# Kernel tuning notes

Hardware: AMD Instinct MI355X
Metric: run time of the kernel (lower is better)

## Reference

```python
import jax, jax.numpy as jnp
import numpy as np

B, N, C = 8, 2048, 512  # batch, points, channels; dk == C


def _mlp(x, W, b):
    # torch MLP helper = Linear followed by ReLU (even on the last layer)
    return jax.nn.relu(x @ W + b)


def setup_inputs() -> dict:
    key = jax.random.key(0)
    ks = jax.random.split(key, 5)
    s = 1.0 / np.sqrt(C)
    return {
        "x": jax.random.normal(ks[0], (B, N, C), dtype=jnp.float32),
        "Wh": jax.random.normal(ks[1], (C, C), dtype=jnp.float32) * s,
        "bh": jnp.zeros((C,), dtype=jnp.float32),
        "Wl": jax.random.normal(ks[2], (C, C), dtype=jnp.float32) * s,
        "bl": jnp.zeros((C,), dtype=jnp.float32),
        "Wg": jax.random.normal(ks[3], (C, C), dtype=jnp.float32) * s,
        "bg": jnp.zeros((C,), dtype=jnp.float32),
        "Wm": jax.random.normal(ks[4], (C, C), dtype=jnp.float32) * s,
        "bm": jnp.zeros((C,), dtype=jnp.float32),
    }


def reference(x, Wh, bh, Wl, bl, Wg, bg, Wm, bm):
    h = _mlp(x, Wh, bh)                      # [B, N, dk] (torch transposes; folded into einsum)
    l = _mlp(x, Wl, bl)                      # [B, N, dk]
    scores = jnp.einsum("bnd,bmd->bnm", l, h)  # [B, N, N]
    attn = jax.nn.softmax(scores, axis=-1)
    g = _mlp(x, Wg, bg)                      # [B, N, C]
    out = x + jnp.einsum("bnm,bmc->bnc", attn, g)
    return _mlp(out, Wm, bm)
```

## Files before the change

### kernel.cpp

```cpp
#include <hip/hip_runtime.h>


typedef __attribute__((ext_vector_type(4))) float f32x4;
typedef __attribute__((ext_vector_type(8))) short s16x8;
typedef __attribute__((ext_vector_type(4))) short s16x4;
typedef __attribute__((ext_vector_type(8))) _Float16 f16x8;
typedef __attribute__((ext_vector_type(4))) _Float16 f16x4;
typedef __attribute__((ext_vector_type(2))) unsigned u32x2;

typedef unsigned int u32;
typedef __attribute__((address_space(1))) const u32 gu32;
typedef __attribute__((address_space(3))) u32 lu32;

__device__ __forceinline__ void gload16(const short* g, short* l) {
  __builtin_amdgcn_global_load_lds((gu32*)g, (lu32*)l, 16, 0, 0);
}

__device__ __forceinline__ short f2h(float f) {
  _Float16 h = (_Float16)f;
  return __builtin_bit_cast(short, h);
}

__device__ __forceinline__ unsigned pk2h(float a, float b) {
  return __builtin_bit_cast(unsigned, __builtin_amdgcn_cvt_pkrtz(a, b));
}

#define MFMA(a, b, c) __builtin_amdgcn_mfma_f32_16x16x32_f16(a, b, c, 0, 0, 0)
#define MFMA16(a, b, c) __builtin_amdgcn_mfma_f32_16x16x16f16(a, b, c, 0, 0, 0)

#define BAR_KEEP2()                                          \
  do {                                                       \
    asm volatile("s_waitcnt vmcnt(2)" ::: "memory");         \
    __builtin_amdgcn_s_barrier();                            \
    __builtin_amdgcn_sched_barrier(0);                       \
  } while (0)
#define BAR_ALL()                                            \
  do {                                                       \
    asm volatile("s_waitcnt vmcnt(0)" ::: "memory");         \
    __builtin_amdgcn_s_barrier();                            \
    __builtin_amdgcn_sched_barrier(0);                       \
  } while (0)


__global__ __launch_bounds__(256) void conv_x_kernel(const float* __restrict__ x,
                                                     short* __restrict__ xb) {
  int i = blockIdx.x * 256 + threadIdx.x;
  const float4* xv = (const float4*)x;
  float4 a = xv[2 * i], b = xv[2 * i + 1];
  s16x8 o;
  o[0] = f2h(a.x); o[1] = f2h(a.y); o[2] = f2h(a.z); o[3] = f2h(a.w);
  o[4] = f2h(b.x); o[5] = f2h(b.y); o[6] = f2h(b.z); o[7] = f2h(b.w);
  ((s16x8*)xb)[i] = o;
}

__global__ __launch_bounds__(256) void conv_w_kernel(const float* __restrict__ Wh,
                                                     const float* __restrict__ Wl,
                                                     const float* __restrict__ Wg,
                                                     const float* __restrict__ Wm,
                                                     short* __restrict__ Wt) {
  int idx = blockIdx.x * 256 + threadIdx.x;
  int k = idx & 511, n = (idx >> 9) & 511, w = idx >> 18;
  const float* W = (w == 0) ? Wh : (w == 1) ? Wl : (w == 2) ? Wg : Wm;
  Wt[idx] = f2h(W[k * 512 + n]);
}


__global__ __launch_bounds__(256) void mlp3_kernel(const short* __restrict__ A,
                                                   const short* __restrict__ Wt_all,
                                                   const float* __restrict__ bh,
                                                   const float* __restrict__ bl,
                                                   const float* __restrict__ bg,
                                                   short* __restrict__ h,
                                                   short* __restrict__ l,
                                                   short* __restrict__ gT) {
  int z = blockIdx.z;
  const short* Wt = Wt_all + z * 262144;
  const float* bias = (z == 0) ? bh : (z == 1) ? bl : bg;

  __shared__ __align__(16) short lds_a[128 * 40];
  __shared__ __align__(16) short lds_b[128 * 40];
  int tid = threadIdx.x, lane = tid & 63, w = tid >> 6;
  int wm = w >> 1, wn = w & 1;
  int bm = blockIdx.x * 128, bn = blockIdx.y * 128;

  f32x4 acc[4][4];
#pragma unroll
  for (int mi = 0; mi < 4; ++mi)
#pragma unroll
    for (int ni = 0; ni < 4; ++ni) acc[mi][ni] = (f32x4){0.f, 0.f, 0.f, 0.f};

  for (int k0 = 0; k0 < 512; k0 += 32) {
#pragma unroll
    for (int it = 0; it < 2; ++it) {
      int chunk = tid + it * 256;
      int row = chunk >> 2, c8 = (chunk & 3) * 8;
      *(s16x8*)&lds_a[row * 40 + c8] =
          *(const s16x8*)&A[(size_t)(bm + row) * 512 + k0 + c8];
      *(s16x8*)&lds_b[row * 40 + c8] =
          *(const s16x8*)&Wt[(bn + row) * 512 + k0 + c8];
    }
    __syncthreads();
    f16x8 af[4], bfr[4];
#pragma unroll
    for (int mi = 0; mi < 4; ++mi)
      af[mi] = *(const f16x8*)&lds_a[(wm * 64 + mi * 16 + (lane & 15)) * 40 +
                                     (lane >> 4) * 8];
#pragma unroll
    for (int ni = 0; ni < 4; ++ni)
      bfr[ni] = *(const f16x8*)&lds_b[(wn * 64 + ni * 16 + (lane & 15)) * 40 +
                                      (lane >> 4) * 8];
#pragma unroll
    for (int mi = 0; mi < 4; ++mi)
#pragma unroll
      for (int ni = 0; ni < 4; ++ni) acc[mi][ni] = MFMA(af[mi], bfr[ni], acc[mi][ni]);
    __syncthreads();
  }

#pragma unroll
  for (int mi = 0; mi < 4; ++mi)
#pragma unroll
    for (int ni = 0; ni < 4; ++ni) {
      int col = bn + wn * 64 + ni * 16 + (lane & 15);
      float bv = bias[col];
#pragma unroll
      for (int r = 0; r < 4; ++r) {
        int row = bm + wm * 64 + mi * 16 + (lane >> 4) * 4 + r;
        float v = fmaxf(acc[mi][ni][r] + bv, 0.0f);
        short o = f2h(v);
        if (z == 0) h[(size_t)row * 512 + col] = o;
        else if (z == 1) l[(size_t)row * 512 + col] = o;
        else {
          int bb = row >> 11, mm = row & 2047;
          gT[((size_t)bb * 512 + col) * 2048 + mm] = o;
        }
      }
    }
}


__global__ __launch_bounds__(512, 1) void attn_split_kernel(
    const short* __restrict__ lmat, const short* __restrict__ hmat,
    const short* __restrict__ gT,
    short* __restrict__ OA, short* __restrict__ OB,
    float2* __restrict__ mlA, float2* __restrict__ mlB) {
  __shared__ __align__(16) short kbuf[3][8192];
  __shared__ __align__(16) short gbuf[2][8192];
  int tid = threadIdx.x, lane = tid & 63, w = tid >> 6;
  int b = blockIdx.x & 7;
  int idx = blockIdx.x >> 3;
  int qt = idx >> 1, sp = idx & 1;
  int q0 = qt * 128 + w * 16;
  int keybase = sp * 1024;
  const short* lb = lmat + (size_t)b * 2048 * 512;
  const short* hb = hmat + (size_t)b * 2048 * 512;
  const short* gb = gT + (size_t)b * 512 * 2048;
  short* Op = sp ? OB : OA;
  float2* ml = sp ? mlB : mlA;

  int r0 = lane & 15, g = lane >> 4;

  f16x8 qf[16];
  {
    int q = q0 + r0;
#pragma unroll
    for (int ks = 0; ks < 16; ++ks)
      qf[ks] = *(const f16x8*)&lb[(size_t)q * 512 + ks * 32 + g * 8];
  }
  f32x4 accO[32];
#pragma unroll
  for (int i = 0; i < 32; ++i) accO[i] = (f32x4){0.f, 0.f, 0.f, 0.f};
  float mrun = -3e38f, lsumL = 0.f;

  auto stageK = [&](int t) {
    int key0 = keybase + t * 16;
    short* kd = &kbuf[t % 3][0];
#pragma unroll
    for (int j = 0; j < 2; ++j) {
      int wl = w * 2 + j;
      gload16(hb + (size_t)(key0 + wl) * 512 + (((lane * 16) ^ ((wl & 7) << 4)) >> 1),
              kd + wl * 512);
    }
  };
  auto stageG = [&](int t) {
    int key0 = keybase + t * 16;
    short* gd = &gbuf[t & 1][0];
#pragma unroll
    for (int j = 0; j < 2; ++j) {
      int wl = w * 2 + j;
      int c = wl * 32 + (lane >> 1);
      int half = (lane & 1) ^ ((lane >> 3) & 1);
      gload16(gb + (size_t)c * 2048 + key0 + half * 8, gd + wl * 512);
    }
  };
  auto QK = [&](int t, f32x4& o) {
    const short* kb = &kbuf[t % 3][0];
#pragma unroll
    for (int ks = 0; ks < 16; ++ks) {
      f16x8 kf = *(const f16x8*)&kb[(r0 * 512 + ks * 32 + g * 8) ^ ((r0 & 7) << 3)];
      o = MFMA(kf, qf[ks], o);
    }
  };

  stageK(0); stageK(1); stageG(0); stageK(2);
  BAR_KEEP2();
  f32x4 sc = {0.f, 0.f, 0.f, 0.f};
  QK(0, sc);
  BAR_KEEP2();

  int goff = r0 * 16 + (((g >> 1) ^ ((r0 >> 2) & 1)) << 3) + ((g & 1) << 2);

  for (int t = 0; t < 64; ++t) {
    if (t < 63) stageG(t + 1);
    if (t < 61) stageK(t + 3);

    f32x4 sn = {0.f, 0.f, 0.f, 0.f};
    if (t < 63) {
      __builtin_amdgcn_s_setprio(1);
      QK(t + 1, sn);
      __builtin_amdgcn_s_setprio(0);
    }

    float m2 = fmaxf(fmaxf(sc[0], sc[1]), fmaxf(sc[2], sc[3]));
    m2 = fmaxf(m2, __shfl_xor(m2, 16));
    m2 = fmaxf(m2, __shfl_xor(m2, 32));
    bool ok = (m2 <= mrun + 8.0f);
    if (!__all((int)ok)) {
      float mnew = fmaxf(mrun, m2);
      float s = __expf(mrun - mnew);
      mrun = mnew;
      lsumL *= s;
#pragma unroll
      for (int nf = 0; nf < 32; ++nf) accO[nf] *= s;
    }
    float p0 = __expf(sc[0] - mrun), p1 = __expf(sc[1] - mrun);
    float p2 = __expf(sc[2] - mrun), p3 = __expf(sc[3] - mrun);
    lsumL += (p0 + p1) + (p2 + p3);

    u32x2 pw = {pk2h(p0, p1), pk2h(p2, p3)};
    f16x4 pfrag = __builtin_bit_cast(f16x4, pw);

    const short* gp = &gbuf[t & 1][goff];
    __builtin_amdgcn_s_setprio(1);
#pragma unroll
    for (int nf = 0; nf < 32; ++nf) {
      f16x4 gf = *(const f16x4*)&gp[nf * 256];
      accO[nf] = MFMA16(gf, pfrag, accO[nf]);
    }
    __builtin_amdgcn_s_setprio(0);

    if (t < 61) BAR_KEEP2(); else BAR_ALL();
    sc = sn;
  }

  float ls = lsumL;
  ls += __shfl_xor(ls, 16);
  ls += __shfl_xor(ls, 32);
  float inv = 1.0f / ls;
  int q = q0 + r0;
#pragma unroll
  for (int nf = 0; nf < 32; ++nf) {
    s16x4 o;
    o[0] = f2h(accO[nf][0] * inv);
    o[1] = f2h(accO[nf][1] * inv);
    o[2] = f2h(accO[nf][2] * inv);
    o[3] = f2h(accO[nf][3] * inv);
    *(s16x4*)&Op[((size_t)b * 2048 + q) * 512 + nf * 16 + g * 4] = o;
  }
  if (g == 0) ml[(size_t)b * 2048 + q] = make_float2(mrun, ls);
}


__global__ __launch_bounds__(256) void final_gemm_kernel(
    const short* __restrict__ OA, const short* __restrict__ OB,
    const float2* __restrict__ mlA, const float2* __restrict__ mlB,
    const float* __restrict__ x, const short* __restrict__ Wt,
    const float* __restrict__ bias, float* __restrict__ out) {
  __shared__ __align__(16) short lds_a[64 * 40];
  __shared__ __align__(16) short lds_b[512 * 40];
  int tid = threadIdx.x, lane = tid & 63, w = tid >> 6;
  int bm = blockIdx.x * 64;

  int arow = tid >> 2, ac8 = (tid & 3) * 8;
  int grow = bm + arow;
  float2 a2 = mlA[grow], b2 = mlB[grow];
  float ms = fmaxf(a2.x, b2.x);
  float wA = __expf(a2.x - ms) * a2.y;
  float wB = __expf(b2.x - ms) * b2.y;
  float winv = 1.0f / (wA + wB);
  wA *= winv; wB *= winv;

  f32x4 acc[32];
#pragma unroll
  for (int i = 0; i < 32; ++i) acc[i] = (f32x4){0.f, 0.f, 0.f, 0.f};

  for (int k0 = 0; k0 < 512; k0 += 32) {
    {
      size_t base = (size_t)grow * 512 + k0 + ac8;
      f16x8 oa = *(const f16x8*)&OA[base];
      f16x8 ob = *(const f16x8*)&OB[base];
      float4 x0 = *(const float4*)&x[base];
      float4 x1 = *(const float4*)&x[base + 4];
      s16x8 av;
      av[0] = f2h((float)oa[0] * wA + (float)ob[0] * wB + x0.x);
      av[1] = f2h((float)oa[1] * wA + (float)ob[1] * wB + x0.y);
      av[2] = f2h((float)oa[2] * wA + (float)ob[2] * wB + x0.z);
      av[3] = f2h((float)oa[3] * wA + (float)ob[3] * wB + x0.w);
      av[4] = f2h((float)oa[4] * wA + (float)ob[4] * wB + x1.x);
      av[5] = f2h((float)oa[5] * wA + (float)ob[5] * wB + x1.y);
      av[6] = f2h((float)oa[6] * wA + (float)ob[6] * wB + x1.z);
      av[7] = f2h((float)oa[7] * wA + (float)ob[7] * wB + x1.w);
      *(s16x8*)&lds_a[arow * 40 + ac8] = av;
    }
#pragma unroll
    for (int it = 0; it < 8; ++it) {
      int chunk = tid + it * 256;
      int row = chunk >> 2, c8 = (chunk & 3) * 8;
      *(s16x8*)&lds_b[row * 40 + c8] =
          *(const s16x8*)&Wt[(size_t)row * 512 + k0 + c8];
    }
    __syncthreads();
    f16x8 af = *(const f16x8*)&lds_a[(w * 16 + (lane & 15)) * 40 + (lane >> 4) * 8];
#pragma unroll
    for (int nf = 0; nf < 32; ++nf) {
      f16x8 bf = *(const f16x8*)&lds_b[(nf * 16 + (lane & 15)) * 40 + (lane >> 4) * 8];
      acc[nf] = MFMA(af, bf, acc[nf]);
    }
    __syncthreads();
  }

#pragma unroll
  for (int nf = 0; nf < 32; ++nf) {
    int col = nf * 16 + (lane & 15);
    float bv = bias[col];
#pragma unroll
    for (int r = 0; r < 4; ++r) {
      int row = bm + w * 16 + (lane >> 4) * 4 + r;
      out[(size_t)row * 512 + col] = fmaxf(acc[nf][r] + bv, 0.0f);
    }
  }
}


extern "C" void kernel_launch(void* const* d_in, const int* in_sizes, int n_in,
                              void* d_out, int out_size, void* d_ws, size_t ws_size,
                              hipStream_t stream) {
  const float* x  = (const float*)d_in[0];
  const float* Wh = (const float*)d_in[1];
  const float* bh = (const float*)d_in[2];
  const float* Wl = (const float*)d_in[3];
  const float* bl = (const float*)d_in[4];
  const float* Wg = (const float*)d_in[5];
  const float* bg = (const float*)d_in[6];
  const float* Wm = (const float*)d_in[7];
  const float* bm = (const float*)d_in[8];

  char* ws = (char*)d_ws;
  const size_t SZ = 16777216;
  short*  xb  = (short*)(ws + 0 * SZ);
  short*  h   = (short*)(ws + 1 * SZ);
  short*  l   = (short*)(ws + 2 * SZ);
  short*  gT  = (short*)(ws + 3 * SZ);
  short*  OB  = (short*)(ws + 4 * SZ);
  short*  Wt  = (short*)(ws + 5 * SZ);
  float2* mlA = (float2*)(ws + 5 * SZ + 2097152);
  float2* mlB = (float2*)(ws + 5 * SZ + 2097152 + 131072);

  conv_x_kernel<<<4096, 256, 0, stream>>>(x, xb);
  conv_w_kernel<<<4096, 256, 0, stream>>>(Wh, Wl, Wg, Wm, Wt);
  mlp3_kernel<<<dim3(128, 4, 3), 256, 0, stream>>>(xb, Wt, bh, bl, bg, h, l, gT);
  attn_split_kernel<<<256, 512, 0, stream>>>(l, h, gT, xb, OB, mlA, mlB);
  final_gemm_kernel<<<256, 256, 0, stream>>>(xb, OB, mlA, mlB, x,
                                             Wt + 3 * 262144, bm, (float*)d_out);
}
```

Baseline: 235.3 us.

## Pipeline MLP and final GEMMs with async LDS loads, swizzle, triple buffering

The projection GEMM now stages its tiles with direct global-to-LDS loads into a triple-buffered, XOR-swizzled LDS layout, replacing the padded synchronous copy and two barriers per k-step. The final GEMM is retiled from 64x512 to 128x128 blocks. Its B tiles are staged asynchronously, and the next A tile (the merged attention output plus residual) is computed in registers while the current step's MFMAs run. The aim is to hide global-memory latency behind compute and reduce barrier stalls. The cost is more LDS, more careful vmcnt/lgkmcnt bookkeeping, and a new grid shape for the final kernel.

```diff
diff --git a/kernel.cpp b/kernel.cpp
--- a/kernel.cpp
+++ b/kernel.cpp
@@ -34,9 +34,21 @@
     __builtin_amdgcn_s_barrier();                            \
     __builtin_amdgcn_sched_barrier(0);                       \
   } while (0)
+#define BAR_KEEP4()                                          \
+  do {                                                       \
+    asm volatile("s_waitcnt vmcnt(4)" ::: "memory");         \
+    __builtin_amdgcn_s_barrier();                            \
+    __builtin_amdgcn_sched_barrier(0);                       \
+  } while (0)
+#define BAR_KEEP4_L()                                        \
+  do {                                                       \
+    asm volatile("s_waitcnt vmcnt(4) lgkmcnt(0)" ::: "memory"); \
+    __builtin_amdgcn_s_barrier();                            \
+    __builtin_amdgcn_sched_barrier(0);                       \
+  } while (0)
 #define BAR_ALL()                                            \
   do {                                                       \
-    asm volatile("s_waitcnt vmcnt(0)" ::: "memory");         \
+    asm volatile("s_waitcnt vmcnt(0) lgkmcnt(0)" ::: "memory"); \
     __builtin_amdgcn_s_barrier();                            \
     __builtin_amdgcn_sched_barrier(0);                       \
   } while (0)
@@ -77,11 +89,27 @@
   const short* Wt = Wt_all + z * 262144;
   const float* bias = (z == 0) ? bh : (z == 1) ? bl : bg;
 
-  __shared__ __align__(16) short lds_a[128 * 40];
-  __shared__ __align__(16) short lds_b[128 * 40];
+  __shared__ __align__(16) short abuf[3][4096];
+  __shared__ __align__(16) short bbuf[3][4096];
   int tid = threadIdx.x, lane = tid & 63, w = tid >> 6;
   int wm = w >> 1, wn = w & 1;
   int bm = blockIdx.x * 128, bn = blockIdx.y * 128;
+  int rx = lane & 15, g = lane >> 4;
+
+  auto stage = [&](int t) {
+    int k0 = t * 32;
+    short* ad = &abuf[t % 3][0];
+    short* bd = &bbuf[t % 3][0];
+    int srow = lane >> 2;
+    int scol = ((lane & 3) ^ ((lane >> 3) & 3)) * 8;
+#pragma unroll
+    for (int j = 0; j < 2; ++j) {
+      int wl = w * 2 + j;
+      int row = wl * 16 + srow;
+      gload16(A + (size_t)(bm + row) * 512 + k0 + scol, ad + wl * 512 + lane * 8);
+      gload16(Wt + (size_t)(bn + row) * 512 + k0 + scol, bd + wl * 512 + lane * 8);
+    }
+  };
 
   f32x4 acc[4][4];
 #pragma unroll
@@ -89,49 +117,46 @@
 #pragma unroll
     for (int ni = 0; ni < 4; ++ni) acc[mi][ni] = (f32x4){0.f, 0.f, 0.f, 0.f};
 
-  for (int k0 = 0; k0 < 512; k0 += 32) {
-#pragma unroll
-    for (int it = 0; it < 2; ++it) {
-      int chunk = tid + it * 256;
-      int row = chunk >> 2, c8 = (chunk & 3) * 8;
-      *(s16x8*)&lds_a[row * 40 + c8] =
-          *(const s16x8*)&A[(size_t)(bm + row) * 512 + k0 + c8];
-      *(s16x8*)&lds_b[row * 40 + c8] =
-          *(const s16x8*)&Wt[(bn + row) * 512 + k0 + c8];
-    }
-    __syncthreads();
+  stage(0); stage(1);
+  BAR_KEEP4();
+
+  int foff = rx * 32 + ((g ^ ((rx >> 1) & 3)) << 3);
+
+  for (int t = 0; t < 16; ++t) {
+    if (t < 14) stage(t + 2);
+    const short* ab = &abuf[t % 3][0];
+    const short* bb = &bbuf[t % 3][0];
     f16x8 af[4], bfr[4];
 #pragma unroll
     for (int mi = 0; mi < 4; ++mi)
-      af[mi] = *(const f16x8*)&lds_a[(wm * 64 + mi * 16 + (lane & 15)) * 40 +
-                                     (lane >> 4) * 8];
+      af[mi] = *(const f16x8*)&ab[(wm * 64 + mi * 16) * 32 + foff];
 #pragma unroll
     for (int ni = 0; ni < 4; ++ni)
-      bfr[ni] = *(const f16x8*)&lds_b[(wn * 64 + ni * 16 + (lane & 15)) * 40 +
-                                      (lane >> 4) * 8];
+      bfr[ni] = *(const f16x8*)&bb[(wn * 64 + ni * 16) * 32 + foff];
 #pragma unroll
     for (int mi = 0; mi < 4; ++mi)
 #pragma unroll
       for (int ni = 0; ni < 4; ++ni) acc[mi][ni] = MFMA(af[mi], bfr[ni], acc[mi][ni]);
-    __syncthreads();
+    if (t < 14) BAR_KEEP4();
+    else if (t == 14) BAR_ALL();
   }
 
 #pragma unroll
   for (int mi = 0; mi < 4; ++mi)
 #pragma unroll
     for (int ni = 0; ni < 4; ++ni) {
-      int col = bn + wn * 64 + ni * 16 + (lane & 15);
+      int col = bn + wn * 64 + ni * 16 + rx;
       float bv = bias[col];
 #pragma unroll
       for (int r = 0; r < 4; ++r) {
-        int row = bm + wm * 64 + mi * 16 + (lane >> 4) * 4 + r;
+        int row = bm + wm * 64 + mi * 16 + g * 4 + r;
         float v = fmaxf(acc[mi][ni][r] + bv, 0.0f);
         short o = f2h(v);
         if (z == 0) h[(size_t)row * 512 + col] = o;
         else if (z == 1) l[(size_t)row * 512 + col] = o;
         else {
-          int bb = row >> 11, mm = row & 2047;
-          gT[((size_t)bb * 512 + col) * 2048 + mm] = o;
+          int bb2 = row >> 11, mm = row & 2047;
+          gT[((size_t)bb2 * 512 + col) * 2048 + mm] = o;
         }
       }
     }
@@ -248,7 +273,12 @@
     }
     __builtin_amdgcn_s_setprio(0);
 
-    if (t < 61) BAR_KEEP2(); else BAR_ALL();
+    if (t < 61) BAR_KEEP2();
+    else {
+      asm volatile("s_waitcnt vmcnt(0)" ::: "memory");
+      __builtin_amdgcn_s_barrier();
+      __builtin_amdgcn_sched_barrier(0);
+    }
     sc = sn;
   }
 
@@ -275,69 +305,119 @@
     const float2* __restrict__ mlA, const float2* __restrict__ mlB,
     const float* __restrict__ x, const short* __restrict__ Wt,
     const float* __restrict__ bias, float* __restrict__ out) {
-  __shared__ __align__(16) short lds_a[64 * 40];
-  __shared__ __align__(16) short lds_b[512 * 40];
+  __shared__ __align__(16) short abuf[2][4096];
+  __shared__ __align__(16) short bbuf[3][4096];
   int tid = threadIdx.x, lane = tid & 63, w = tid >> 6;
-  int bm = blockIdx.x * 64;
-
-  int arow = tid >> 2, ac8 = (tid & 3) * 8;
-  int grow = bm + arow;
-  float2 a2 = mlA[grow], b2 = mlB[grow];
-  float ms = fmaxf(a2.x, b2.x);
-  float wA = __expf(a2.x - ms) * a2.y;
-  float wB = __expf(b2.x - ms) * b2.y;
-  float winv = 1.0f / (wA + wB);
-  wA *= winv; wB *= winv;
-
-  f32x4 acc[32];
-#pragma unroll
-  for (int i = 0; i < 32; ++i) acc[i] = (f32x4){0.f, 0.f, 0.f, 0.f};
-
-  for (int k0 = 0; k0 < 512; k0 += 32) {
-    {
-      size_t base = (size_t)grow * 512 + k0 + ac8;
+  int wm = w >> 1, wn = w & 1;
+  int bm = blockIdx.x * 128, bn = blockIdx.y * 128;
+  int rx = lane & 15, g = lane >> 4;
+
+  float wgt[2][2];
+#pragma unroll
+  for (int it = 0; it < 2; ++it) {
+    int row = (tid >> 2) + it * 64;
+    float2 a2 = mlA[bm + row], b2 = mlB[bm + row];
+    float ms = fmaxf(a2.x, b2.x);
+    float wA = __expf(a2.x - ms) * a2.y;
+    float wB = __expf(b2.x - ms) * b2.y;
+    float winv = 1.0f / (wA + wB);
+    wgt[it][0] = wA * winv;
+    wgt[it][1] = wB * winv;
+  }
+
+  auto stageB = [&](int t) {
+    int k0 = t * 32;
+    short* bd = &bbuf[t % 3][0];
+    int srow = lane >> 2;
+    int scol = ((lane & 3) ^ ((lane >> 3) & 3)) * 8;
+#pragma unroll
+    for (int j = 0; j < 2; ++j) {
+      int wl = w * 2 + j;
+      int row = wl * 16 + srow;
+      gload16(Wt + (size_t)(bn + row) * 512 + k0 + scol, bd + wl * 512 + lane * 8);
+    }
+  };
+  auto loadA = [&](int t, s16x8 av[2]) {
+#pragma unroll
+    for (int it = 0; it < 2; ++it) {
+      int c = tid + it * 256;
+      int row = c >> 2, col8 = (c & 3) * 8;
+      size_t base = (size_t)(bm + row) * 512 + t * 32 + col8;
       f16x8 oa = *(const f16x8*)&OA[base];
       f16x8 ob = *(const f16x8*)&OB[base];
       float4 x0 = *(const float4*)&x[base];
       float4 x1 = *(const float4*)&x[base + 4];
-      s16x8 av;
-      av[0] = f2h((float)oa[0] * wA + (float)ob[0] * wB + x0.x);
-      av[1] = f2h((float)oa[1] * wA + (float)ob[1] * wB + x0.y);
-      av[2] = f2h((float)oa[2] * wA + (float)ob[2] * wB + x0.z);
-      av[3] = f2h((float)oa[3] * wA + (float)ob[3] * wB + x0.w);
-      av[4] = f2h((float)oa[4] * wA + (float)ob[4] * wB + x1.x);
-      av[5] = f2h((float)oa[5] * wA + (float)ob[5] * wB + x1.y);
-      av[6] = f2h((float)oa[6] * wA + (float)ob[6] * wB + x1.z);
-      av[7] = f2h((float)oa[7] * wA + (float)ob[7] * wB + x1.w);
-      *(s16x8*)&lds_a[arow * 40 + ac8] = av;
-    }
-#pragma unroll
-    for (int it = 0; it < 8; ++it) {
-      int chunk = tid + it * 256;
-      int row = chunk >> 2, c8 = (chunk & 3) * 8;
-      *(s16x8*)&lds_b[row * 40 + c8] =
-          *(const s16x8*)&Wt[(size_t)row * 512 + k0 + c8];
-    }
-    __syncthreads();
-    f16x8 af = *(const f16x8*)&lds_a[(w * 16 + (lane & 15)) * 40 + (lane >> 4) * 8];
-#pragma unroll
-    for (int nf = 0; nf < 32; ++nf) {
-      f16x8 bf = *(const f16x8*)&lds_b[(nf * 16 + (lane & 15)) * 40 + (lane >> 4) * 8];
-      acc[nf] = MFMA(af, bf, acc[nf]);
-    }
-    __syncthreads();
-  }
-
-#pragma unroll
-  for (int nf = 0; nf < 32; ++nf) {
-    int col = nf * 16 + (lane & 15);
-    float bv = bias[col];
-#pragma unroll
-    for (int r = 0; r < 4; ++r) {
-      int row = bm + w * 16 + (lane >> 4) * 4 + r;
-      out[(size_t)row * 512 + col] = fmaxf(acc[nf][r] + bv, 0.0f);
-    }
-  }
+      float wA = wgt[it][0], wB = wgt[it][1];
+      s16x8 v;
+      v[0] = f2h((float)oa[0] * wA + (float)ob[0] * wB + x0.x);
+      v[1] = f2h((float)oa[1] * wA + (float)ob[1] * wB + x0.y);
+      v[2] = f2h((float)oa[2] * wA + (float)ob[2] * wB + x0.z);
+      v[3] = f2h((float)oa[3] * wA + (float)ob[3] * wB + x0.w);
+      v[4] = f2h((float)oa[4] * wA + (float)ob[4] * wB + x1.x);
+      v[5] = f2h((float)oa[5] * wA + (float)ob[5] * wB + x1.y);
+      v[6] = f2h((float)oa[6] * wA + (float)ob[6] * wB + x1.z);
+      v[7] = f2h((float)oa[7] * wA + (float)ob[7] * wB + x1.w);
+      av[it] = v;
+    }
+  };
+  auto writeA = [&](int t, s16x8 av[2]) {
+    short* ad = &abuf[t & 1][0];
+#pragma unroll
+    for (int it = 0; it < 2; ++it) {
+      int c = tid + it * 256;
+      int row = c >> 2;
+      int chunk_p = (c & 3) ^ ((row >> 1) & 3);
+      *(s16x8*)&ad[row * 32 + chunk_p * 8] = av[it];
+    }
+  };
+
+  f32x4 acc[4][4];
+#pragma unroll
+  for (int mi = 0; mi < 4; ++mi)
+#pragma unroll
+    for (int ni = 0; ni < 4; ++ni) acc[mi][ni] = (f32x4){0.f, 0.f, 0.f, 0.f};
+
+  s16x8 av[2];
+  loadA(0, av);
+  stageB(0); stageB(1);
+  writeA(0, av);
+  BAR_KEEP4_L();
+
+  int foff = rx * 32 + ((g ^ ((rx >> 1) & 3)) << 3);
+
+  for (int t = 0; t < 16; ++t) {
+    if (t < 15) loadA(t + 1, av);
+    if (t < 14) stageB(t + 2);
+    const short* ab = &abuf[t & 1][0];
+    const short* bb = &bbuf[t % 3][0];
+    f16x8 af[4], bfr[4];
+#pragma unroll
+    for (int mi = 0; mi < 4; ++mi)
+      af[mi] = *(const f16x8*)&ab[(wm * 64 + mi * 16) * 32 + foff];
+#pragma unroll
+    for (int ni = 0; ni < 4; ++ni)
+      bfr[ni] = *(const f16x8*)&bb[(wn * 64 + ni * 16) * 32 + foff];
+#pragma unroll
+    for (int mi = 0; mi < 4; ++mi)
+#pragma unroll
+      for (int ni = 0; ni < 4; ++ni) acc[mi][ni] = MFMA(af[mi], bfr[ni], acc[mi][ni]);
+    if (t < 15) writeA(t + 1, av);
+    if (t < 14) BAR_KEEP4_L();
+    else if (t == 14) BAR_ALL();
+  }
+
+#pragma unroll
+  for (int mi = 0; mi < 4; ++mi)
+#pragma unroll
+    for (int ni = 0; ni < 4; ++ni) {
+      int col = bn + wn * 64 + ni * 16 + rx;
+      float bv = bias[col];
+#pragma unroll
+      for (int r = 0; r < 4; ++r) {
+        int row = bm + wm * 64 + mi * 16 + g * 4 + r;
+        out[(size_t)row * 512 + col] = fmaxf(acc[mi][ni][r] + bv, 0.0f);
+      }
+    }
 }
 
 
@@ -369,6 +449,7 @@
   conv_w_kernel<<<4096, 256, 0, stream>>>(Wh, Wl, Wg, Wm, Wt);
   mlp3_kernel<<<dim3(128, 4, 3), 256, 0, stream>>>(xb, Wt, bh, bl, bg, h, l, gT);
   attn_split_kernel<<<256, 512, 0, stream>>>(l, h, gT, xb, OB, mlA, mlB);
-  final_gemm_kernel<<<256, 256, 0, stream>>>(xb, OB, mlA, mlB, x,
-                                             Wt + 3 * 262144, bm, (float*)d_out);
-}
+  final_gemm_kernel<<<dim3(128, 4), 256, 0, stream>>>(xb, OB, mlA, mlB, x,
+                                                      Wt + 3 * 262144, bm,
+                                                      (float*)d_out);
+}
```

Result: no change. 231.5 us (-1.6%).
